# Performance work log

Hardware: AMD Instinct MI355X
Metric: run time of the kernel (lower is better)

The kernel has to match this reference:

```python
import jax, jax.numpy as jnp
import numpy as np

B, H, S, DK = 2, 16, 2048, 64


def setup_inputs() -> dict:
    key = jax.random.key(0)
    kq, kk, kv = jax.random.split(key, 3)
    q = jax.random.normal(kq, (B, H, S, DK), dtype=jnp.float32)
    k = jax.random.normal(kk, (B, H, S, DK), dtype=jnp.float32)
    v = jax.random.normal(kv, (B, H, S, DK), dtype=jnp.float32)
    # 3-D boolean mask [B, Sq, Sk]; True = allowed. Causal lower-triangular.
    mask = jnp.broadcast_to(jnp.tril(jnp.ones((S, S), dtype=bool)), (B, S, S))
    return {"q": q, "k": k, "v": v, "mask": mask}


def reference(q, k, v, mask):
    # scores: [B, H, Sq, Sk]
    scores = jnp.einsum("bhqd,bhkd->bhqk", q, k) / jnp.sqrt(jnp.asarray(DK, q.dtype))
    if mask.ndim == scores.ndim - 1:
        mask = mask[:, None, :, :]  # broadcast over heads
    scores = jnp.where(mask, scores, jnp.asarray(-jnp.inf, scores.dtype))
    attn = jax.nn.softmax(scores, axis=-1)
    out = jnp.einsum("bhqk,bhkd->bhqd", attn, v)
    return out
```

## Files before the change

kernel.cpp:

```cpp
#include <hip/hip_runtime.h>


typedef float    v4f __attribute__((ext_vector_type(4)));
typedef _Float16 v4h __attribute__((ext_vector_type(4)));
typedef _Float16 v8h __attribute__((ext_vector_type(8)));

#define SEQ 2048
#define DKC 64

#if __has_builtin(__builtin_amdgcn_exp2f)
#define EXP2(x) __builtin_amdgcn_exp2f(x)
#else
#define EXP2(x) exp2f(x)
#endif

#define MFMA16(a,b,c) __builtin_amdgcn_mfma_f32_16x16x16f16(a,b,c,0,0,0)
#define MFMA32(a,b,c) __builtin_amdgcn_mfma_f32_16x16x32_f16(a,b,c,0,0,0)

__global__ __launch_bounds__(256) void prep_kv(const float* __restrict__ k,
                                               const float* __restrict__ v,
                                               _Float16* __restrict__ kh,
                                               _Float16* __restrict__ vt) {
  const int bh = blockIdx.x;
  const int kt = blockIdx.y;
  const int tid = threadIdx.x;
  {
    const int quad = tid & 3;
    const int l16  = (tid >> 2) & 15;
    const int st   = (tid >> 6) & 1;
    const int s    = tid >> 7;
    const float* src = k + ((size_t)bh * SEQ + kt * 32 + s * 16 + l16) * DKC + st * 32 + quad * 8;
    float4 a = *(const float4*)src;
    float4 b = *(const float4*)(src + 4);
    v8h h;
    h[0] = (_Float16)a.x; h[1] = (_Float16)a.y; h[2] = (_Float16)a.z; h[3] = (_Float16)a.w;
    h[4] = (_Float16)b.x; h[5] = (_Float16)b.y; h[6] = (_Float16)b.z; h[7] = (_Float16)b.w;
    *(v8h*)(kh + (size_t)bh * SEQ * DKC
               + (size_t)(kt * 4 + s * 2 + st) * 512 + (quad * 16 + l16) * 8) = h;
  }
  {
    const int d = tid & 63, q4 = tid >> 6;
    const float* src = v + ((size_t)bh * SEQ + kt * 32) * DKC + d;
    v8h h;
#pragma unroll
    for (int j = 0; j < 4; ++j) h[j]     = (_Float16)src[(size_t)(q4 * 4 + j) * DKC];
#pragma unroll
    for (int j = 0; j < 4; ++j) h[4 + j] = (_Float16)src[(size_t)(16 + q4 * 4 + j) * DKC];
    *(v8h*)(vt + (size_t)bh * SEQ * DKC + (size_t)kt * 2048
               + (d >> 4) * 512 + (q4 * 16 + (d & 15)) * 8) = h;
  }
}

__device__ __forceinline__ void compute_chunk(int k0, bool straddle, int qw, int l16, int quad,
                                              const v8h (&qf)[2][2],
                                              const v8h (&kf)[4], const v8h (&va)[4],
                                              v4f (&O)[2][4], v4f (&L)[2], const v4h ones) {
  v4f S[2][2] = {};
#pragma unroll
  for (int t = 0; t < 2; ++t)
#pragma unroll
    for (int s = 0; s < 2; ++s) {
      S[t][s] = MFMA32(kf[s * 2 + 0], qf[t][0], S[t][s]);
      S[t][s] = MFMA32(kf[s * 2 + 1], qf[t][1], S[t][s]);
    }

  if (straddle) {
#pragma unroll
    for (int t = 0; t < 2; ++t) {
      const int qg = qw + t * 16 + l16;
#pragma unroll
      for (int s = 0; s < 2; ++s) {
        const int kb = k0 + s * 16 + quad * 4;
#pragma unroll
        for (int r = 0; r < 4; ++r)
          if (kb + r > qg) S[t][s][r] = -3e38f;
      }
    }
  }

  v4h pf[2][2];
#pragma unroll
  for (int t = 0; t < 2; ++t)
#pragma unroll
    for (int s = 0; s < 2; ++s) {
      v4h p;
#pragma unroll
      for (int r = 0; r < 4; ++r) p[r] = (_Float16)EXP2(S[t][s][r]);
      pf[t][s] = p;
    }

#pragma unroll
  for (int dc = 0; dc < 4; ++dc) {
    v4h lo = __builtin_shufflevector(va[dc], va[dc], 0, 1, 2, 3);
    v4h hi = __builtin_shufflevector(va[dc], va[dc], 4, 5, 6, 7);
    O[0][dc] = MFMA16(lo, pf[0][0], O[0][dc]);
    O[0][dc] = MFMA16(hi, pf[0][1], O[0][dc]);
    O[1][dc] = MFMA16(lo, pf[1][0], O[1][dc]);
    O[1][dc] = MFMA16(hi, pf[1][1], O[1][dc]);
  }
  L[0] = MFMA16(ones, pf[0][0], L[0]);
  L[0] = MFMA16(ones, pf[0][1], L[0]);
  L[1] = MFMA16(ones, pf[1][0], L[1]);
  L[1] = MFMA16(ones, pf[1][1], L[1]);
}

#define GLD16(gp, lp) __builtin_amdgcn_global_load_lds(                     \
    (const __attribute__((address_space(1))) void*)(gp),                    \
    (__attribute__((address_space(3))) void*)(lp), 16, 0, 0)

#define STAGE(bf, c) do {                                                   \
    const char* _gk = khb + (size_t)(c) * 16384 + wv * 2048 + lane * 16;    \
    const char* _gv = vtb + (size_t)(c) * 16384 + wv * 2048 + lane * 16;    \
    char* _lk = ((char*)&lds[bf][0][0]) + wv * 2048;                        \
    char* _lv = ((char*)&lds[bf][1][0]) + wv * 2048;                        \
    GLD16(_gk, _lk); GLD16(_gk + 1024, _lk + 1024);                         \
    GLD16(_gv, _lv); GLD16(_gv + 1024, _lv + 1024);                         \
  } while (0)

__global__ __launch_bounds__(512) void fa_fwd(const float* __restrict__ q,
                                              const _Float16* __restrict__ kh,
                                              const _Float16* __restrict__ vt,
                                              float* __restrict__ out) {
  __shared__ _Float16 lds[2][2][8192];

  const int lane = threadIdx.x & 63;
  const int wv   = threadIdx.x >> 6;
  const int w    = wv & 3;
  const int grp  = wv >> 2;
  const int quad = lane >> 4;
  const int l16  = lane & 15;

  const int g  = (int)blockIdx.x & 7;
  const int r  = (int)blockIdx.x >> 3;
  const int bh = g * 4 + (r & 3);
  const int p  = r >> 2;

  const size_t base = (size_t)bh * SEQ * DKC;
  const char* khb = (const char*)(kh + base);
  const char* vtb = (const char*)(vt + base);

  const float CSC = 0.18033688011112042f;
  const v4h ones = {(_Float16)1.f, (_Float16)1.f, (_Float16)1.f, (_Float16)1.f};

  const int qwA  = p * 128 + w * 32;
  const int qwB  = (15 - p) * 128 + w * 32;
  const int mykA = 4 * p + w;
  const int mykB = 4 * (15 - p) + w;
  const int NC   = 16 - p;

  v8h qfA[2][2], qfB[2][2];
#pragma unroll
  for (int t = 0; t < 2; ++t)
#pragma unroll
    for (int st = 0; st < 2; ++st) {
      const float* qrA = q + base + (size_t)(qwA + t * 16 + l16) * DKC + st * 32 + quad * 8;
      const float* qrB = q + base + (size_t)(qwB + t * 16 + l16) * DKC + st * 32 + quad * 8;
      float4 a = *(const float4*)qrA;
      float4 b = *(const float4*)(qrA + 4);
      v8h hq;
      hq[0] = (_Float16)(a.x * CSC); hq[1] = (_Float16)(a.y * CSC);
      hq[2] = (_Float16)(a.z * CSC); hq[3] = (_Float16)(a.w * CSC);
      hq[4] = (_Float16)(b.x * CSC); hq[5] = (_Float16)(b.y * CSC);
      hq[6] = (_Float16)(b.z * CSC); hq[7] = (_Float16)(b.w * CSC);
      qfA[t][st] = hq;
      a = *(const float4*)qrB;
      b = *(const float4*)(qrB + 4);
      hq[0] = (_Float16)(a.x * CSC); hq[1] = (_Float16)(a.y * CSC);
      hq[2] = (_Float16)(a.z * CSC); hq[3] = (_Float16)(a.w * CSC);
      hq[4] = (_Float16)(b.x * CSC); hq[5] = (_Float16)(b.y * CSC);
      hq[6] = (_Float16)(b.z * CSC); hq[7] = (_Float16)(b.w * CSC);
      qfB[t][st] = hq;
    }

  v4f OA[2][4] = {}, OB[2][4] = {};
  v4f LA[2] = {}, LB[2] = {};

  STAGE(0, 0);
  __syncthreads();

  for (int c = 0; c < NC; ++c) {
    if (c + 1 < NC) STAGE((c + 1) & 1, c + 1);
    const int b = c & 1;
#pragma unroll
    for (int kl = 0; kl < 4; ++kl) {
      if ((kl & 1) != grp) continue;
      const int kt32 = c * 4 + kl;
      if (kt32 <= mykB) {
        v8h kf[4], va[4];
#pragma unroll
        for (int i = 0; i < 4; ++i) kf[i] = *(const v8h*)&lds[b][0][kl * 2048 + i * 512 + lane * 8];
#pragma unroll
        for (int i = 0; i < 4; ++i) va[i] = *(const v8h*)&lds[b][1][kl * 2048 + i * 512 + lane * 8];
        if (kt32 <= mykA)
          compute_chunk(kt32 * 32, kt32 == mykA, qwA, l16, quad, qfA, kf, va, OA, LA, ones);
        compute_chunk(kt32 * 32, kt32 == mykB, qwB, l16, quad, qfB, kf, va, OB, LB, ones);
      }
    }
    __syncthreads();
  }

  v4f (*cb)[64] = (v4f(*)[64])&lds[0][0][0];

  if (!grp) {
#pragma unroll
    for (int t = 0; t < 2; ++t) {
#pragma unroll
      for (int dc = 0; dc < 4; ++dc) cb[w * 10 + t * 4 + dc][lane] = OA[t][dc];
      cb[w * 10 + 8 + t][lane] = LA[t];
    }
  }
  __syncthreads();
  if (grp) {
#pragma unroll
    for (int t = 0; t < 2; ++t) {
#pragma unroll
      for (int dc = 0; dc < 4; ++dc) OA[t][dc] += cb[w * 10 + t * 4 + dc][lane];
      LA[t] += cb[w * 10 + 8 + t][lane];
    }
#pragma unroll
    for (int t = 0; t < 2; ++t) {
      const float inv = 1.0f / LA[t][0];
      float* orow = out + base + (size_t)(qwA + t * 16 + l16) * DKC + quad * 4;
#pragma unroll
      for (int dc = 0; dc < 4; ++dc) {
        float4 o;
        o.x = OA[t][dc][0] * inv; o.y = OA[t][dc][1] * inv;
        o.z = OA[t][dc][2] * inv; o.w = OA[t][dc][3] * inv;
        *(float4*)(orow + dc * 16) = o;
      }
    }
  }
  __syncthreads();

  if (grp) {
#pragma unroll
    for (int t = 0; t < 2; ++t) {
#pragma unroll
      for (int dc = 0; dc < 4; ++dc) cb[w * 10 + t * 4 + dc][lane] = OB[t][dc];
      cb[w * 10 + 8 + t][lane] = LB[t];
    }
  }
  __syncthreads();
  if (!grp) {
#pragma unroll
    for (int t = 0; t < 2; ++t) {
#pragma unroll
      for (int dc = 0; dc < 4; ++dc) OB[t][dc] += cb[w * 10 + t * 4 + dc][lane];
      LB[t] += cb[w * 10 + 8 + t][lane];
    }
#pragma unroll
    for (int t = 0; t < 2; ++t) {
      const float inv = 1.0f / LB[t][0];
      float* orow = out + base + (size_t)(qwB + t * 16 + l16) * DKC + quad * 4;
#pragma unroll
      for (int dc = 0; dc < 4; ++dc) {
        float4 o;
        o.x = OB[t][dc][0] * inv; o.y = OB[t][dc][1] * inv;
        o.z = OB[t][dc][2] * inv; o.w = OB[t][dc][3] * inv;
        *(float4*)(orow + dc * 16) = o;
      }
    }
  }
}

extern "C" void kernel_launch(void* const* d_in, const int* in_sizes, int n_in,
                              void* d_out, int out_size, void* d_ws, size_t ws_size,
                              hipStream_t stream) {
  (void)in_sizes; (void)n_in; (void)out_size; (void)ws_size;
  const float* q = (const float*)d_in[0];
  const float* k = (const float*)d_in[1];
  const float* v = (const float*)d_in[2];
  float* out = (float*)d_out;

  _Float16* kh = (_Float16*)d_ws;
  _Float16* vt = (_Float16*)((char*)d_ws + (size_t)32 * SEQ * DKC * 2);

  prep_kv<<<dim3(32, 64), dim3(256), 0, stream>>>(k, v, kh, vt);
  fa_fwd<<<dim3(256), dim3(512), 0, stream>>>(q, kh, vt, out);
}
```

Measured before the change: 137.3 us.

## Split key chunks across four wave groups with 1024-thread blocks

Doubles the block to 16 waves so each of four wave groups processes one 32-key subtile per staged chunk, instead of two groups each handling two subtiles. Staging is spread across twice as many waves, each issuing half the loads. The final cross-group reduction now sums three partial accumulators through a larger LDS buffer. The aim is more in-flight waves to hide latency, at the cost of higher register pressure under 1024-thread launch bounds, more LDS, and a larger reduction.

New measurement: 230.7 us. +68.0%, slower.

```diff
diff --git a/kernel.cpp b/kernel.cpp
--- a/kernel.cpp
+++ b/kernel.cpp
@@ -109,19 +109,21 @@
     (__attribute__((address_space(3))) void*)(lp), 16, 0, 0)
 
 #define STAGE(bf, c) do {                                                   \
-    const char* _gk = khb + (size_t)(c) * 16384 + wv * 2048 + lane * 16;    \
-    const char* _gv = vtb + (size_t)(c) * 16384 + wv * 2048 + lane * 16;    \
-    char* _lk = ((char*)&lds[bf][0][0]) + wv * 2048;                        \
-    char* _lv = ((char*)&lds[bf][1][0]) + wv * 2048;                        \
-    GLD16(_gk, _lk); GLD16(_gk + 1024, _lk + 1024);                         \
-    GLD16(_gv, _lv); GLD16(_gv + 1024, _lv + 1024);                         \
+    const char* _gk = khb + (size_t)(c) * 16384 + wv * 1024 + lane * 16;    \
+    const char* _gv = vtb + (size_t)(c) * 16384 + wv * 1024 + lane * 16;    \
+    char* _lk = ((char*)&lds[bf][0][0]) + wv * 1024;                        \
+    char* _lv = ((char*)&lds[bf][1][0]) + wv * 1024;                        \
+    GLD16(_gk, _lk);                                                        \
+    GLD16(_gv, _lv);                                                        \
   } while (0)
 
-__global__ __launch_bounds__(512) void fa_fwd(const float* __restrict__ q,
-                                              const _Float16* __restrict__ kh,
-                                              const _Float16* __restrict__ vt,
-                                              float* __restrict__ out) {
-  __shared__ _Float16 lds[2][2][8192];
+__global__ __launch_bounds__(1024) void fa_fwd(const float* __restrict__ q,
+                                               const _Float16* __restrict__ kh,
+                                               const _Float16* __restrict__ vt,
+                                               float* __restrict__ out) {
+  __shared__ __align__(16) char smem[122880];
+  _Float16 (*lds)[2][8192] = reinterpret_cast<_Float16(*)[2][8192]>(smem);
+  v4f (*cb)[4][10][64]     = reinterpret_cast<v4f(*)[4][10][64]>(smem);
 
   const int lane = threadIdx.x & 63;
   const int wv   = threadIdx.x >> 6;
@@ -181,42 +183,38 @@
   for (int c = 0; c < NC; ++c) {
     if (c + 1 < NC) STAGE((c + 1) & 1, c + 1);
     const int b = c & 1;
-#pragma unroll
-    for (int kl = 0; kl < 4; ++kl) {
-      if ((kl & 1) != grp) continue;
-      const int kt32 = c * 4 + kl;
-      if (kt32 <= mykB) {
-        v8h kf[4], va[4];
-#pragma unroll
-        for (int i = 0; i < 4; ++i) kf[i] = *(const v8h*)&lds[b][0][kl * 2048 + i * 512 + lane * 8];
-#pragma unroll
-        for (int i = 0; i < 4; ++i) va[i] = *(const v8h*)&lds[b][1][kl * 2048 + i * 512 + lane * 8];
-        if (kt32 <= mykA)
-          compute_chunk(kt32 * 32, kt32 == mykA, qwA, l16, quad, qfA, kf, va, OA, LA, ones);
-        compute_chunk(kt32 * 32, kt32 == mykB, qwB, l16, quad, qfB, kf, va, OB, LB, ones);
-      }
+    const int kt32 = c * 4 + grp;
+    if (kt32 <= mykB) {
+      v8h kf[4], va[4];
+#pragma unroll
+      for (int i = 0; i < 4; ++i) kf[i] = *(const v8h*)&lds[b][0][grp * 2048 + i * 512 + lane * 8];
+#pragma unroll
+      for (int i = 0; i < 4; ++i) va[i] = *(const v8h*)&lds[b][1][grp * 2048 + i * 512 + lane * 8];
+      if (kt32 <= mykA)
+        compute_chunk(kt32 * 32, kt32 == mykA, qwA, l16, quad, qfA, kf, va, OA, LA, ones);
+      compute_chunk(kt32 * 32, kt32 == mykB, qwB, l16, quad, qfB, kf, va, OB, LB, ones);
     }
     __syncthreads();
   }
 
-  v4f (*cb)[64] = (v4f(*)[64])&lds[0][0][0];
-
-  if (!grp) {
-#pragma unroll
-    for (int t = 0; t < 2; ++t) {
-#pragma unroll
-      for (int dc = 0; dc < 4; ++dc) cb[w * 10 + t * 4 + dc][lane] = OA[t][dc];
-      cb[w * 10 + 8 + t][lane] = LA[t];
-    }
-  }
-  __syncthreads();
-  if (grp) {
-#pragma unroll
-    for (int t = 0; t < 2; ++t) {
-#pragma unroll
-      for (int dc = 0; dc < 4; ++dc) OA[t][dc] += cb[w * 10 + t * 4 + dc][lane];
-      LA[t] += cb[w * 10 + 8 + t][lane];
-    }
+  if (grp >= 1) {
+#pragma unroll
+    for (int t = 0; t < 2; ++t) {
+#pragma unroll
+      for (int dc = 0; dc < 4; ++dc) cb[grp - 1][w][t * 4 + dc][lane] = OA[t][dc];
+      cb[grp - 1][w][8 + t][lane] = LA[t];
+    }
+  }
+  __syncthreads();
+  if (grp == 0) {
+#pragma unroll
+    for (int s = 0; s < 3; ++s)
+#pragma unroll
+      for (int t = 0; t < 2; ++t) {
+#pragma unroll
+        for (int dc = 0; dc < 4; ++dc) OA[t][dc] += cb[s][w][t * 4 + dc][lane];
+        LA[t] += cb[s][w][8 + t][lane];
+      }
 #pragma unroll
     for (int t = 0; t < 2; ++t) {
       const float inv = 1.0f / LA[t][0];
@@ -232,22 +230,25 @@
   }
   __syncthreads();
 
-  if (grp) {
-#pragma unroll
-    for (int t = 0; t < 2; ++t) {
-#pragma unroll
-      for (int dc = 0; dc < 4; ++dc) cb[w * 10 + t * 4 + dc][lane] = OB[t][dc];
-      cb[w * 10 + 8 + t][lane] = LB[t];
-    }
-  }
-  __syncthreads();
-  if (!grp) {
-#pragma unroll
-    for (int t = 0; t < 2; ++t) {
-#pragma unroll
-      for (int dc = 0; dc < 4; ++dc) OB[t][dc] += cb[w * 10 + t * 4 + dc][lane];
-      LB[t] += cb[w * 10 + 8 + t][lane];
-    }
+  if (grp != 1) {
+    const int s = (grp == 0) ? 0 : grp - 1;
+#pragma unroll
+    for (int t = 0; t < 2; ++t) {
+#pragma unroll
+      for (int dc = 0; dc < 4; ++dc) cb[s][w][t * 4 + dc][lane] = OB[t][dc];
+      cb[s][w][8 + t][lane] = LB[t];
+    }
+  }
+  __syncthreads();
+  if (grp == 1) {
+#pragma unroll
+    for (int s = 0; s < 3; ++s)
+#pragma unroll
+      for (int t = 0; t < 2; ++t) {
+#pragma unroll
+        for (int dc = 0; dc < 4; ++dc) OB[t][dc] += cb[s][w][t * 4 + dc][lane];
+        LB[t] += cb[s][w][8 + t][lane];
+      }
 #pragma unroll
     for (int t = 0; t < 2; ++t) {
       const float inv = 1.0f / LB[t][0];
@@ -276,5 +277,5 @@
   _Float16* vt = (_Float16*)((char*)d_ws + (size_t)32 * SEQ * DKC * 2);
 
   prep_kv<<<dim3(32, 64), dim3(256), 0, stream>>>(k, v, kh, vt);
-  fa_fwd<<<dim3(256), dim3(512), 0, stream>>>(q, kh, vt, out);
-}
+  fa_fwd<<<dim3(256), dim3(1024), 0, stream>>>(q, kh, vt, out);
+}
```
